# Optimization experiments

Hardware: AMD Instinct MI355X
Metric: run time of the kernel (lower is better)

Reference implementation:

```python
import jax, jax.numpy as jnp
import numpy as np

N_HEADS = 16


def setup_inputs() -> dict:
    key = jax.random.key(0)
    ks = jax.random.split(key, 9)
    B, S, D = 2, 2048, 1024
    sc = 0.02
    return {
        'x': jax.random.normal(ks[0], (B, S, D), jnp.float32),
        'Wq': jax.random.normal(ks[1], (D, D), jnp.float32) * sc,
        'bq': jax.random.normal(ks[2], (D,), jnp.float32) * sc,
        'Wk': jax.random.normal(ks[3], (D, D), jnp.float32) * sc,
        'bk': jax.random.normal(ks[4], (D,), jnp.float32) * sc,
        'Wv': jax.random.normal(ks[5], (D, D), jnp.float32) * sc,
        'bv': jax.random.normal(ks[6], (D,), jnp.float32) * sc,
        'Wo': jax.random.normal(ks[7], (D, D), jnp.float32) * sc,
        'bo': jax.random.normal(ks[8], (D,), jnp.float32) * sc,
    }


def reference(x, Wq, bq, Wk, bk, Wv, bv, Wo, bo):
    # Chunked causal prefill. The chunk-wise mask (q_pos >= kv_pos over the
    # growing KV cache) is mathematically identical to full causal attention,
    # so we compute it as one vectorized masked softmax attention.
    B, S, D = x.shape
    H = N_HEADS
    hd = D // H

    def proj(W, b):
        # torch Linear: y = x @ W.T + b ; then split heads -> [B,H,S,hd]
        y = jnp.einsum('bsd,ed->bse', x, W) + b
        return y.reshape(B, S, H, hd).transpose(0, 2, 1, 3)

    q = proj(Wq, bq)
    k = proj(Wk, bk)
    v = proj(Wv, bv)

    scores = jnp.einsum('bhqd,bhkd->bhqk', q, k) / jnp.sqrt(jnp.asarray(hd, x.dtype))
    causal = jnp.tril(jnp.ones((S, S), dtype=bool))  # [S,S]
    scores = jnp.where(causal[None, None], scores, jnp.asarray(-jnp.inf, scores.dtype))
    attn = jax.nn.softmax(scores, axis=-1)
    ctx = jnp.einsum('bhqk,bhkd->bhqd', attn, v)  # [B,H,S,hd]
    ctx = ctx.transpose(0, 2, 1, 3).reshape(B, S, D)
    out = jnp.einsum('bsd,ed->bse', ctx, Wo) + bo
    return out
```

## Files before the change

### kernel.cpp

```cpp
#include <hip/hip_runtime.h>
#include <cstdint>
#include <math.h>

typedef _Float16 f16;
typedef _Float16 f16x2 __attribute__((ext_vector_type(2)));
typedef _Float16 f16x4 __attribute__((ext_vector_type(4)));
typedef _Float16 f16x8 __attribute__((ext_vector_type(8)));
typedef __fp16   h16x2 __attribute__((ext_vector_type(2)));
typedef float    f32x4 __attribute__((ext_vector_type(4)));

__device__ __forceinline__ f32x4 mfma16(f16x8 a, f16x8 b, f32x4 c) {
  return __builtin_amdgcn_mfma_f32_16x16x32_f16(a, b, c, 0, 0, 0);
}
__device__ __forceinline__ void gl2lds16(const f16* g, f16* l) {
  __builtin_amdgcn_global_load_lds((__attribute__((address_space(1))) void*)(g),
                                   (__attribute__((address_space(3))) void*)(l),
                                   16, 0, 0);
}
__device__ __forceinline__ float fexp2(float x) { return __builtin_amdgcn_exp2f(x); }
__device__ __forceinline__ f16x2 pkrtz(float a, float b) {
  h16x2 r = __builtin_amdgcn_cvt_pkrtz(a, b);
  return __builtin_bit_cast(f16x2, r);
}
__device__ __forceinline__ float dot2acc(f16x2 a, f16x2 b, float c) {
#if __has_builtin(__builtin_amdgcn_fdot2)
  return __builtin_amdgcn_fdot2(__builtin_bit_cast(h16x2, a),
                                __builtin_bit_cast(h16x2, b), c, false);
#else
  return c + (float)a[0] * (float)b[0] + (float)a[1] * (float)b[1];
#endif
}

__global__ __launch_bounds__(256) void cvt_kernel(
    const float* __restrict__ x,  const float* __restrict__ wq, const float* __restrict__ wk,
    const float* __restrict__ wv, const float* __restrict__ wo,
    f16* __restrict__ xh, f16* __restrict__ wqkvh, f16* __restrict__ woh)
{
  const int blk = blockIdx.x;
  const float* src; f16* dst; int off;
  if (blk < 2048)      { src = x;  dst = xh;              off = blk; }
  else {
    const int wseg = (blk - 2048) >> 9;
    off = (blk - 2048) & 511;
    if      (wseg == 0) { src = wq; dst = wqkvh; }
    else if (wseg == 1) { src = wk; dst = wqkvh + 1048576; }
    else if (wseg == 2) { src = wv; dst = wqkvh + 2097152; }
    else                { src = wo; dst = woh; }
  }
  const int idx = off * 2048 + (int)threadIdx.x * 8;
  f32x4 a = *(const f32x4*)(src + idx);
  f32x4 b = *(const f32x4*)(src + idx + 4);
  f16x8 h;
  h[0] = (f16)a[0]; h[1] = (f16)a[1]; h[2] = (f16)a[2]; h[3] = (f16)a[3];
  h[4] = (f16)b[0]; h[5] = (f16)b[1]; h[6] = (f16)b[2]; h[7] = (f16)b[3];
  *(f16x8*)(dst + idx) = h;
}

__global__ __launch_bounds__(256) void gemm_qkv(
    const f16* __restrict__ A, const f16* __restrict__ B,
    const float* __restrict__ bias0, const float* __restrict__ bias1, const float* __restrict__ bias2,
    f16* __restrict__ Qp, f16* __restrict__ Kp, f16* __restrict__ Vtp)
{
  constexpr int K = 1024;
  __shared__ __align__(16) f16 As[2][128 * 32];
  __shared__ __align__(16) f16 Bs[2][128 * 32];
  const int tid  = threadIdx.x;
  const int wave = tid >> 6, lane = tid & 63;
  const int quad = lane >> 4, col = lane & 15;
  const int tile_m = blockIdx.y * 128, tile_n = blockIdx.x * 128;
  const int mb = (wave >> 1) * 64, nb = (wave & 1) * 64;
  const int srow = lane >> 2, scol = (lane & 3) * 8;
  const f16* gA = A + (size_t)(tile_m + wave * 32 + srow) * K + scol;
  const f16* gB = B + (size_t)(tile_n + wave * 32 + srow) * K + scol;

  auto stage = [&](int buf, int k0) {
    gl2lds16(gA + k0,          &As[buf][wave * 1024]);
    gl2lds16(gA + 16 * K + k0, &As[buf][wave * 1024 + 512]);
    gl2lds16(gB + k0,          &Bs[buf][wave * 1024]);
    gl2lds16(gB + 16 * K + k0, &Bs[buf][wave * 1024 + 512]);
  };

  f32x4 acc[4][4] = {};
  stage(0, 0);
  for (int k0 = 0; k0 < K; k0 += 32) {
    const int cur = (k0 >> 5) & 1;
    __syncthreads();
    if (k0 + 32 < K) stage(cur ^ 1, k0 + 32);
    f16x8 af[4], bf[4];
    #pragma unroll
    for (int i = 0; i < 4; ++i)
      af[i] = *(const f16x8*)&As[cur][(mb + i * 16 + col) * 32 + quad * 8];
    #pragma unroll
    for (int j = 0; j < 4; ++j)
      bf[j] = *(const f16x8*)&Bs[cur][(nb + j * 16 + col) * 32 + quad * 8];
    #pragma unroll
    for (int i = 0; i < 4; ++i)
      #pragma unroll
      for (int j = 0; j < 4; ++j)
        acc[i][j] = mfma16(af[i], bf[j], acc[i][j]);
  }

  #pragma unroll
  for (int j = 0; j < 4; ++j) {
    const int gn = tile_n + nb + j * 16 + col;
    const int which = gn >> 10;
    const int d = gn & 1023;
    const int h = d >> 6, hi = d & 63;
    if (which == 2) {
      const float bvv = bias2[d];
      #pragma unroll
      for (int i = 0; i < 4; ++i) {
        const int gm = tile_m + mb + i * 16 + quad * 4;
        const int bb = gm >> 11, s = gm & 2047;
        f16x4 pw;
        #pragma unroll
        for (int r = 0; r < 4; ++r) pw[r] = (f16)(acc[i][j][r] + bvv);
        *(f16x4*)&Vtp[(((size_t)bb * 16 + h) * 64 + hi) * 2048 + s] = pw;
      }
    } else {
      const float* bp = (which == 0) ? bias0 : bias1;
      f16* dst        = (which == 0) ? Qp    : Kp;
      const float bvv = bp[d];
      const float qs  = (which == 0) ? 0.18033688f : 1.0f;
      #pragma unroll
      for (int i = 0; i < 4; ++i) {
        #pragma unroll
        for (int r = 0; r < 4; ++r) {
          const int gm = tile_m + mb + i * 16 + quad * 4 + r;
          const int bb = gm >> 11, s = gm & 2047;
          dst[(((size_t)bb * 16 + h) * 2048 + s) * 64 + hi] = (f16)((acc[i][j][r] + bvv) * qs);
        }
      }
    }
  }
}

__global__ __launch_bounds__(256, 4) void attn_kernel(
    const f16* __restrict__ Q, const f16* __restrict__ K, const f16* __restrict__ Vt,
    f16* __restrict__ ctx)
{
  __shared__ __align__(16) f16 Ks[2][64 * 72];
  __shared__ __align__(16) f16 Vts[2][64 * 72];
  __shared__ __align__(16) f16 Ps[4][2][16 * 72];

  const int bh  = blockIdx.x;
  const int yy  = blockIdx.y;
  const int p   = (yy < 8) ? yy : 23 - yy;
  const int qlong = 31 - p, qshort = p;
  const int tid = threadIdx.x;
  const int wave = tid >> 6, lane = tid & 63;
  const int quad = lane >> 4, col = lane & 15;
  const int b = bh >> 4, h = bh & 15;
  const size_t base = (size_t)bh * 2048 * 64;
  const size_t vtb  = (size_t)bh * 64 * 2048;

  int srow[2], sc8[2];
  #pragma unroll
  for (int i = 0; i < 2; ++i) {
    const int flat = tid + i * 256;
    srow[i] = flat >> 3;
    sc8[i]  = (flat & 7) * 8;
  }

  const int qa = qlong * 64 + wave * 16;
  const int qb = qshort * 64 + wave * 16;
  const f16x8 bqa0 = *(const f16x8*)&Q[base + (size_t)(qa + col) * 64 + quad * 8];
  const f16x8 bqa1 = *(const f16x8*)&Q[base + (size_t)(qa + col) * 64 + 32 + quad * 8];
  const f16x8 bqb0 = *(const f16x8*)&Q[base + (size_t)(qb + col) * 64 + quad * 8];
  const f16x8 bqb1 = *(const f16x8*)&Q[base + (size_t)(qb + col) * 64 + 32 + quad * 8];

  f32x4 cta[4] = {}, ctb[4] = {};
  float la = 0.f, lb2 = 0.f;

  f16x8 kr[2], vr[2];
  auto gload = [&](int t) {
    #pragma unroll
    for (int i = 0; i < 2; ++i) {
      kr[i] = *(const f16x8*)&K[base + (size_t)(t * 64 + srow[i]) * 64 + sc8[i]];
      vr[i] = *(const f16x8*)&Vt[vtb + (size_t)srow[i] * 2048 + t * 64 + sc8[i]];
    }
  };
  auto swrite = [&](int buf) {
    #pragma unroll
    for (int i = 0; i < 2; ++i) {
      *(f16x8*)&Ks[buf][srow[i] * 72 + sc8[i]]  = kr[i];
      *(f16x8*)&Vts[buf][srow[i] * 72 + sc8[i]] = vr[i];
    }
  };

  const int nIter = qlong + 1;

  gload(0);
  __syncthreads();
  swrite(0);
  gload(1);

  for (int t = 0; t < nIter; ++t) {
    const int cur = t & 1;
    __syncthreads();
    if (t + 1 < nIter) {
      swrite(cur ^ 1);
      if (t + 2 < nIter) gload(t + 2);
    }
    const bool doB = (t <= qshort);

    f32x4 sa[4], sb[4];
    __builtin_amdgcn_s_setprio(1);
    #pragma unroll
    for (int jt = 0; jt < 4; ++jt) {
      const int kro = (jt * 16 + col) * 72;
      const f16x8 ak0 = *(const f16x8*)&Ks[cur][kro + quad * 8];
      const f16x8 ak1 = *(const f16x8*)&Ks[cur][kro + 32 + quad * 8];
      f32x4 za = {};
      za = mfma16(ak0, bqa0, za);
      sa[jt] = mfma16(ak1, bqa1, za);
      if (doB) {
        f32x4 zb = {};
        zb = mfma16(ak0, bqb0, zb);
        sb[jt] = mfma16(ak1, bqb1, zb);
      }
    }
    __builtin_amdgcn_s_setprio(0);

    if (t == qlong) {
      #pragma unroll
      for (int jt = 0; jt < 4; ++jt) {
        const int kg = t * 64 + jt * 16 + quad * 4;
        #pragma unroll
        for (int r = 0; r < 4; ++r)
          if (kg + r > qa + col) sa[jt][r] = -1e30f;
      }
    }
    if (t == qshort) {
      #pragma unroll
      for (int jt = 0; jt < 4; ++jt) {
        const int kg = t * 64 + jt * 16 + quad * 4;
        #pragma unroll
        for (int r = 0; r < 4; ++r)
          if (kg + r > qb + col) sb[jt][r] = -1e30f;
      }
    }

    const f16x2 one2 = {(_Float16)1.f, (_Float16)1.f};

    {
      float rs = 0.f;
      #pragma unroll
      for (int jt = 0; jt < 4; ++jt) {
        const f16x2 a01 = pkrtz(fexp2(sa[jt][0]), fexp2(sa[jt][1]));
        const f16x2 a23 = pkrtz(fexp2(sa[jt][2]), fexp2(sa[jt][3]));
        rs = dot2acc(a01, one2, rs);
        rs = dot2acc(a23, one2, rs);
        f16x4 pw; pw[0] = a01[0]; pw[1] = a01[1]; pw[2] = a23[0]; pw[3] = a23[1];
        *(f16x4*)&Ps[wave][0][col * 72 + jt * 16 + quad * 4] = pw;
      }
      la += rs;
    }

    if (doB) {
      float rs = 0.f;
      #pragma unroll
      for (int jt = 0; jt < 4; ++jt) {
        const f16x2 a01 = pkrtz(fexp2(sb[jt][0]), fexp2(sb[jt][1]));
        const f16x2 a23 = pkrtz(fexp2(sb[jt][2]), fexp2(sb[jt][3]));
        rs = dot2acc(a01, one2, rs);
        rs = dot2acc(a23, one2, rs);
        f16x4 pw; pw[0] = a01[0]; pw[1] = a01[1]; pw[2] = a23[0]; pw[3] = a23[1];
        *(f16x4*)&Ps[wave][1][col * 72 + jt * 16 + quad * 4] = pw;
      }
      lb2 += rs;
    }

    __asm__ volatile("s_waitcnt lgkmcnt(0)" ::: "memory");

    const f16x8 apa0 = *(const f16x8*)&Ps[wave][0][col * 72 + quad * 8];
    const f16x8 apa1 = *(const f16x8*)&Ps[wave][0][col * 72 + 32 + quad * 8];
    __builtin_amdgcn_s_setprio(1);
    if (doB) {
      const f16x8 apb0 = *(const f16x8*)&Ps[wave][1][col * 72 + quad * 8];
      const f16x8 apb1 = *(const f16x8*)&Ps[wave][1][col * 72 + 32 + quad * 8];
      #pragma unroll
      for (int jd = 0; jd < 4; ++jd) {
        const int vro = (jd * 16 + col) * 72;
        const f16x8 bv0 = *(const f16x8*)&Vts[cur][vro + quad * 8];
        const f16x8 bv1 = *(const f16x8*)&Vts[cur][vro + 32 + quad * 8];
        cta[jd] = mfma16(apa1, bv1, mfma16(apa0, bv0, cta[jd]));
        ctb[jd] = mfma16(apb1, bv1, mfma16(apb0, bv0, ctb[jd]));
      }
    } else {
      #pragma unroll
      for (int jd = 0; jd < 4; ++jd) {
        const int vro = (jd * 16 + col) * 72;
        const f16x8 bv0 = *(const f16x8*)&Vts[cur][vro + quad * 8];
        const f16x8 bv1 = *(const f16x8*)&Vts[cur][vro + 32 + quad * 8];
        cta[jd] = mfma16(apa1, bv1, mfma16(apa0, bv0, cta[jd]));
      }
    }
    __builtin_amdgcn_s_setprio(0);
  }

  {
    la += __shfl_xor(la, 16);
    la += __shfl_xor(la, 32);
    f32x4 lva;
    #pragma unroll
    for (int r = 0; r < 4; ++r) lva[r] = __shfl(la, quad * 4 + r);
    #pragma unroll
    for (int jd = 0; jd < 4; ++jd) {
      #pragma unroll
      for (int r = 0; r < 4; ++r) {
        const int qga = qa + quad * 4 + r;
        const int d = h * 64 + jd * 16 + col;
        ctx[((size_t)b * 2048 + qga) * 1024 + d] = (f16)(cta[jd][r] / lva[r]);
      }
    }
  }
  {
    lb2 += __shfl_xor(lb2, 16);
    lb2 += __shfl_xor(lb2, 32);
    f32x4 lvb;
    #pragma unroll
    for (int r = 0; r < 4; ++r) lvb[r] = __shfl(lb2, quad * 4 + r);
    #pragma unroll
    for (int jd = 0; jd < 4; ++jd) {
      #pragma unroll
      for (int r = 0; r < 4; ++r) {
        const int qgb = qb + quad * 4 + r;
        const int d = h * 64 + jd * 16 + col;
        ctx[((size_t)b * 2048 + qgb) * 1024 + d] = (f16)(ctb[jd][r] / lvb[r]);
      }
    }
  }
}

__global__ __launch_bounds__(256) void gemm_o(
    const f16* __restrict__ A, const f16* __restrict__ B, const float* __restrict__ bias,
    float* __restrict__ Out)
{
  constexpr int K = 1024;
  __shared__ __align__(16) f16 As[2][2][128 * 32];
  __shared__ __align__(16) f16 Bs[2][2][64 * 32];
  const int tid  = threadIdx.x;
  const int wave = tid >> 6, lane = tid & 63;
  const int quad = lane >> 4, col = lane & 15;
  const int tile_m = blockIdx.y * 128, tile_n = blockIdx.x * 64;
  const int mb = wave * 32;
  const int srow = lane >> 2, scol = (lane & 3) * 8;
  const f16* gA = A + (size_t)(tile_m + srow) * K + scol;
  const f16* gB = B + (size_t)(tile_n + srow) * K + scol;

  auto stage = [&](int buf, int k0) {
    #pragma unroll
    for (int ks = 0; ks < 2; ++ks) {
      #pragma unroll
      for (int i = 0; i < 2; ++i)
        gl2lds16(gA + (size_t)(wave * 32 + i * 16) * K + k0 + ks * 32,
                 &As[buf][ks][(wave * 32 + i * 16) * 32]);
      gl2lds16(gB + (size_t)(wave * 16) * K + k0 + ks * 32,
               &Bs[buf][ks][(wave * 16) * 32]);
    }
  };

  f32x4 acc[2][4] = {};
  stage(0, 0);
  for (int k0 = 0; k0 < K; k0 += 64) {
    const int cur = (k0 >> 6) & 1;
    __syncthreads();
    if (k0 + 64 < K) stage(cur ^ 1, k0 + 64);
    #pragma unroll
    for (int ks = 0; ks < 2; ++ks) {
      f16x8 af[2], bf[4];
      #pragma unroll
      for (int i = 0; i < 2; ++i)
        af[i] = *(const f16x8*)&As[cur][ks][(mb + i * 16 + col) * 32 + quad * 8];
      #pragma unroll
      for (int j = 0; j < 4; ++j)
        bf[j] = *(const f16x8*)&Bs[cur][ks][(j * 16 + col) * 32 + quad * 8];
      #pragma unroll
      for (int i = 0; i < 2; ++i)
        #pragma unroll
        for (int j = 0; j < 4; ++j)
          acc[i][j] = mfma16(af[i], bf[j], acc[i][j]);
    }
  }

  #pragma unroll
  for (int j = 0; j < 4; ++j) {
    const int gn = tile_n + j * 16 + col;
    const float bvv = bias[gn];
    #pragma unroll
    for (int i = 0; i < 2; ++i) {
      #pragma unroll
      for (int r = 0; r < 4; ++r) {
        const int gm = tile_m + mb + i * 16 + quad * 4 + r;
        Out[(size_t)gm * 1024 + gn] = acc[i][j][r] + bvv;
      }
    }
  }
}

extern "C" void kernel_launch(void* const* d_in, const int* in_sizes, int n_in,
                              void* d_out, int out_size, void* d_ws, size_t ws_size,
                              hipStream_t stream)
{
  const float* x  = (const float*)d_in[0];
  const float* Wq = (const float*)d_in[1];
  const float* bq = (const float*)d_in[2];
  const float* Wk = (const float*)d_in[3];
  const float* bk = (const float*)d_in[4];
  const float* Wv = (const float*)d_in[5];
  const float* bv = (const float*)d_in[6];
  const float* Wo = (const float*)d_in[7];
  const float* bo = (const float*)d_in[8];
  float* out = (float*)d_out;

  f16* ws = (f16*)d_ws;
  const size_t M1 = 1048576;
  f16* xh    = ws;
  f16* wqkvh = ws + 4  * M1;
  f16* woh   = ws + 7  * M1;
  f16* Qh    = ws + 8  * M1;
  f16* Kh    = ws + 12 * M1;
  f16* Vth   = ws + 20 * M1;
  f16* ctxh  = ws + 24 * M1;

  cvt_kernel<<<4096, 256, 0, stream>>>(x, Wq, Wk, Wv, Wo, xh, wqkvh, woh);
  gemm_qkv<<<dim3(24, 32), 256, 0, stream>>>(xh, wqkvh, bq, bk, bv, Qh, Kh, Vth);
  attn_kernel<<<dim3(32, 16), 256, 0, stream>>>(Qh, Kh, Vth, ctxh);
  gemm_o<<<dim3(16, 32), 256, 0, stream>>>(ctxh, woh, bo, out);
}
```

Measured before the change: 184.9 us.

## Store Q transposed for vectorized epilogue writes and delay K/V staging in attention

```diff
diff --git a/kernel.cpp b/kernel.cpp
--- a/kernel.cpp
+++ b/kernel.cpp
@@ -59,7 +59,7 @@
 __global__ __launch_bounds__(256) void gemm_qkv(
     const f16* __restrict__ A, const f16* __restrict__ B,
     const float* __restrict__ bias0, const float* __restrict__ bias1, const float* __restrict__ bias2,
-    f16* __restrict__ Qp, f16* __restrict__ Kp, f16* __restrict__ Vtp)
+    f16* __restrict__ Qtp, f16* __restrict__ Kp, f16* __restrict__ Vtp)
 {
   constexpr int K = 1024;
   __shared__ __align__(16) f16 As[2][128 * 32];
@@ -106,29 +106,29 @@
     const int which = gn >> 10;
     const int d = gn & 1023;
     const int h = d >> 6, hi = d & 63;
-    if (which == 2) {
-      const float bvv = bias2[d];
+    if (which != 1) {
+      const float* bp = (which == 0) ? bias0 : bias2;
+      f16* dst        = (which == 0) ? Qtp  : Vtp;
+      const float bvv = bp[d];
+      const float qs  = (which == 0) ? 0.18033688f : 1.0f;
       #pragma unroll
       for (int i = 0; i < 4; ++i) {
         const int gm = tile_m + mb + i * 16 + quad * 4;
         const int bb = gm >> 11, s = gm & 2047;
         f16x4 pw;
         #pragma unroll
-        for (int r = 0; r < 4; ++r) pw[r] = (f16)(acc[i][j][r] + bvv);
-        *(f16x4*)&Vtp[(((size_t)bb * 16 + h) * 64 + hi) * 2048 + s] = pw;
+        for (int r = 0; r < 4; ++r) pw[r] = (f16)((acc[i][j][r] + bvv) * qs);
+        *(f16x4*)&dst[(((size_t)bb * 16 + h) * 64 + hi) * 2048 + s] = pw;
       }
     } else {
-      const float* bp = (which == 0) ? bias0 : bias1;
-      f16* dst        = (which == 0) ? Qp    : Kp;
-      const float bvv = bp[d];
-      const float qs  = (which == 0) ? 0.18033688f : 1.0f;
+      const float bvv = bias1[d];
       #pragma unroll
       for (int i = 0; i < 4; ++i) {
         #pragma unroll
         for (int r = 0; r < 4; ++r) {
           const int gm = tile_m + mb + i * 16 + quad * 4 + r;
           const int bb = gm >> 11, s = gm & 2047;
-          dst[(((size_t)bb * 16 + h) * 2048 + s) * 64 + hi] = (f16)((acc[i][j][r] + bvv) * qs);
+          Kp[(((size_t)bb * 16 + h) * 2048 + s) * 64 + hi] = (f16)(acc[i][j][r] + bvv);
         }
       }
     }
@@ -136,7 +136,7 @@
 }
 
 __global__ __launch_bounds__(256, 4) void attn_kernel(
-    const f16* __restrict__ Q, const f16* __restrict__ K, const f16* __restrict__ Vt,
+    const f16* __restrict__ Qt, const f16* __restrict__ K, const f16* __restrict__ Vt,
     f16* __restrict__ ctx)
 {
   __shared__ __align__(16) f16 Ks[2][64 * 72];
@@ -164,10 +164,16 @@
 
   const int qa = qlong * 64 + wave * 16;
   const int qb = qshort * 64 + wave * 16;
-  const f16x8 bqa0 = *(const f16x8*)&Q[base + (size_t)(qa + col) * 64 + quad * 8];
-  const f16x8 bqa1 = *(const f16x8*)&Q[base + (size_t)(qa + col) * 64 + 32 + quad * 8];
-  const f16x8 bqb0 = *(const f16x8*)&Q[base + (size_t)(qb + col) * 64 + quad * 8];
-  const f16x8 bqb1 = *(const f16x8*)&Q[base + (size_t)(qb + col) * 64 + 32 + quad * 8];
+  f16x8 bqa0, bqa1, bqb0, bqb1;
+  #pragma unroll
+  for (int j = 0; j < 8; ++j) {
+    const size_t r0 = vtb + (size_t)(quad * 8 + j) * 2048;
+    const size_t r1 = vtb + (size_t)(32 + quad * 8 + j) * 2048;
+    bqa0[j] = Qt[r0 + qa + col];
+    bqa1[j] = Qt[r1 + qa + col];
+    bqb0[j] = Qt[r0 + qb + col];
+    bqb1[j] = Qt[r1 + qb + col];
+  }
 
   f32x4 cta[4] = {}, ctb[4] = {};
   float la = 0.f, lb2 = 0.f;
@@ -198,10 +204,6 @@
   for (int t = 0; t < nIter; ++t) {
     const int cur = t & 1;
     __syncthreads();
-    if (t + 1 < nIter) {
-      swrite(cur ^ 1);
-      if (t + 2 < nIter) gload(t + 2);
-    }
     const bool doB = (t <= qshort);
 
     f32x4 sa[4], sb[4];
@@ -275,6 +277,12 @@
 
     const f16x8 apa0 = *(const f16x8*)&Ps[wave][0][col * 72 + quad * 8];
     const f16x8 apa1 = *(const f16x8*)&Ps[wave][0][col * 72 + 32 + quad * 8];
+
+    if (t + 1 < nIter) {
+      swrite(cur ^ 1);
+      if (t + 2 < nIter) gload(t + 2);
+    }
+
     __builtin_amdgcn_s_setprio(1);
     if (doB) {
       const f16x8 apb0 = *(const f16x8*)&Ps[wave][1][col * 72 + quad * 8];
@@ -419,13 +427,13 @@
   f16* xh    = ws;
   f16* wqkvh = ws + 4  * M1;
   f16* woh   = ws + 7  * M1;
-  f16* Qh    = ws + 8  * M1;
+  f16* Qth   = ws + 8  * M1;
   f16* Kh    = ws + 12 * M1;
   f16* Vth   = ws + 20 * M1;
   f16* ctxh  = ws + 24 * M1;
 
   cvt_kernel<<<4096, 256, 0, stream>>>(x, Wq, Wk, Wv, Wo, xh, wqkvh, woh);
-  gemm_qkv<<<dim3(24, 32), 256, 0, stream>>>(xh, wqkvh, bq, bk, bv, Qh, Kh, Vth);
-  attn_kernel<<<dim3(32, 16), 256, 0, stream>>>(Qh, Kh, Vth, ctxh);
+  gemm_qkv<<<dim3(24, 32), 256, 0, stream>>>(xh, wqkvh, bq, bk, bv, Qth, Kh, Vth);
+  attn_kernel<<<dim3(32, 16), 256, 0, stream>>>(Qth, Kh, Vth, ctxh);
   gemm_o<<<dim3(16, 32), 256, 0, stream>>>(ctxh, woh, bo, out);
 }
```

Result: no change. 185.0 us (+0.1%).
